# Kernel optimization log

Hardware: AMD Instinct MI355X
Metric: run time of the kernel (lower is better)

## Reference

```python
import jax, jax.numpy as jnp
import numpy as np

EPSILON = 0.3
ALPHA = 0.7
LN_EPS = 1e-5


def _layernorm(x, g, b):
    mu = jnp.mean(x, axis=-1, keepdims=True)
    var = jnp.mean((x - mu) ** 2, axis=-1, keepdims=True)
    return (x - mu) / jnp.sqrt(var + LN_EPS) * g + b


def setup_inputs() -> dict:
    key = jax.random.key(0)
    ks = jax.random.split(key, 6)
    B, N, D, L = 1, 2048, 768, 16
    s = 0.05  # weight scale to keep sigmoid/exp well-conditioned
    return {
        "x": jax.random.normal(ks[0], (B, N, D), jnp.float32),
        "proj_w": jax.random.normal(ks[1], (D, L), jnp.float32) * s,
        "proj_b": jnp.zeros((L,), jnp.float32),
        "ln1_g": jnp.ones((L,), jnp.float32),
        "ln1_b": jnp.zeros((L,), jnp.float32),
        "pi_w1": jax.random.normal(ks[2], (L, D), jnp.float32) * s,
        "pi_b1": jnp.zeros((D,), jnp.float32),
        "pi_w2": jax.random.normal(ks[3], (D, 1), jnp.float32) * s,
        "pi_b2": jnp.zeros((1,), jnp.float32),
        "dt": jnp.full((1,), 0.05, jnp.float32),
        "f_w": jax.random.normal(ks[4], (D, D), jnp.float32) * s,
        "f_b": jnp.zeros((D,), jnp.float32),
        "ln2_g": jnp.ones((D,), jnp.float32),
        "ln2_b": jnp.zeros((D,), jnp.float32),
    }


def reference(x, proj_w, proj_b, ln1_g, ln1_b, pi_w1, pi_b1, pi_w2, pi_b2, dt, f_w, f_b, ln2_g, ln2_b):
    B, N, D = x.shape
    # proj_list: Linear -> LayerNorm -> ReLU. [B,N,L]
    x_proj = jax.nn.relu(_layernorm(x @ proj_w + proj_b, ln1_g, ln1_b))
    # RBF kernel over pairwise differences. [B,N,N]
    diff = x_proj[:, :, None, :] - x_proj[:, None, :, :]
    K_eps = jnp.exp(-(1.0 / (4.0 * EPSILON)) * jnp.sum(diff * diff, axis=-1))
    q_tilde = jnp.sum(K_eps, axis=2)  # [B,N]
    # pi_list: Linear -> ReLU -> Linear -> Sigmoid. [B,N]
    pi = jax.nn.sigmoid(jax.nn.relu(x_proj @ pi_w1 + pi_b1) @ pi_w2 + pi_b2)[..., 0]
    v = pi / q_tilde  # diagonal of D_epsilon_tilde
    # K_tilde = K_eps @ diag(v): column scaling (math-equivalent to bmm with diag_embed)
    K_tilde = K_eps * v[:, None, :]
    d = jnp.sum(K_tilde, axis=2) + 1e-5  # diagonal of D_tilde
    # inv(D_tilde) @ K_tilde: row scaling; then subtract identity
    L_op = (1.0 / EPSILON) * (K_tilde / d[:, :, None]) - jnp.eye(N, dtype=x.dtype)[None]
    L_mat = L_op[0]  # .squeeze(0), B == 1
    # f(x): modeled as linear map
    target = x @ f_w + f_b  # [B,N,D]
    tt = dt * jnp.einsum('ij,bjd->bid', L_mat, target)  # target_transformed
    target1 = target + tt
    target2 = ALPHA * x + (1.0 - ALPHA) * (target1 + tt)
    return _layernorm(target2, ln2_g, ln2_b)
```

## Files before the change

kernel.cpp:

```cpp
#include <hip/hip_runtime.h>
#include <math.h>

#define EPSILON 0.3f
#define ALPHA 0.7f
#define LN_EPS 1e-5f

typedef __bf16 bf16x8 __attribute__((ext_vector_type(8)));
typedef float f32x4 __attribute__((ext_vector_type(4)));

__device__ __forceinline__ unsigned short f2bf(float f) {
  unsigned int u = __float_as_uint(f);
  return (unsigned short)((u + 0x7fffu + ((u >> 16) & 1u)) >> 16);
}
__device__ __forceinline__ unsigned int pack2(float lo, float hi) {
  return (unsigned int)f2bf(lo) | ((unsigned int)f2bf(hi) << 16);
}

__device__ __forceinline__ void async16(const unsigned short* g,
                                        unsigned short* l) {
  __builtin_amdgcn_global_load_lds(
      (const __attribute__((address_space(1))) unsigned int*)g,
      (__attribute__((address_space(3))) unsigned int*)l, 16, 0, 0);
}

__device__ __forceinline__ float wave_reduce(float v) {
#pragma unroll
  for (int off = 32; off > 0; off >>= 1) v += __shfl_xor(v, off, 64);
  return v;
}

__device__ __forceinline__ float blk_reduce_sum(float v, float* red) {
  v = wave_reduce(v);
  int lane = threadIdx.x & 63, wid = threadIdx.x >> 6;
  __syncthreads();
  if (lane == 0) red[wid] = v;
  __syncthreads();
  float s = 0.f;
  int nw = (blockDim.x + 63) >> 6;
  for (int w = 0; w < nw; ++w) s += red[w];
  return s;
}

__global__ __launch_bounds__(256) void k_proj(
    const float* __restrict__ x, const float* __restrict__ proj_w,
    const float* __restrict__ proj_b, const float* __restrict__ ln1_g,
    const float* __restrict__ ln1_b, const float* __restrict__ pi_w1,
    const float* __restrict__ pi_b1, const float* __restrict__ pi_w2,
    const float* __restrict__ pi_b2, const float* __restrict__ fw,
    unsigned short* __restrict__ fwTb, float* __restrict__ xp,
    float* __restrict__ s, float* __restrict__ pi, int N, int D) {
  __shared__ float xs[16][68];
  __shared__ float ws[64][20];
  __shared__ float ysh[16][17];
  __shared__ float xps[16][16];
  __shared__ float pr[16][4];
  int tid = threadIdx.x;
  int nProj = N / 16;
  if (blockIdx.x >= (unsigned)nProj) {
    unsigned short(*tile)[33] = (unsigned short(*)[33])&ws[0][0];
    int t = blockIdx.x - nProj;
    int tx = tid & 31, ty = tid >> 5;
    int cols = D / 32;
    int c0 = (t % cols) * 32, r0 = (t / cols) * 32;
#pragma unroll
    for (int i = 0; i < 4; ++i) {
      int r = r0 + ty + i * 8;
      tile[ty + i * 8][tx] = f2bf(fw[(size_t)r * D + c0 + tx]);
    }
    __syncthreads();
#pragma unroll
    for (int i = 0; i < 4; ++i) {
      int cc = c0 + ty + i * 8;
      fwTb[(size_t)cc * D + r0 + tx] = tile[tx][ty + i * 8];
    }
    return;
  }
  int row0 = blockIdx.x * 16;
  int row = tid >> 4, l = tid & 15;
  int lane = tid & 63, w = tid >> 6;
  int skc = (tid & 15) * 4;
  int wk = tid >> 2, wl = (tid & 3) * 4;
  float acc = 0.f;
  for (int k0 = 0; k0 < D; k0 += 64) {
    float4 xv = *(const float4*)(x + (size_t)(row0 + row) * D + k0 + skc);
    float4 wv = *(const float4*)(proj_w + (size_t)(k0 + wk) * 16 + wl);
    __syncthreads();
    *(float4*)&xs[row][skc] = xv;
    *(float4*)&ws[wk][wl] = wv;
    __syncthreads();
#pragma unroll
    for (int kk = 0; kk < 64; kk += 4) {
      float4 a4 = *(const float4*)&xs[row][kk];
      acc += a4.x * ws[kk + 0][l];
      acc += a4.y * ws[kk + 1][l];
      acc += a4.z * ws[kk + 2][l];
      acc += a4.w * ws[kk + 3][l];
    }
  }
  float y = acc + proj_b[l];
  ysh[row][l] = y;
  __syncthreads();
  float mu = 0.f;
#pragma unroll
  for (int t = 0; t < 16; ++t) mu += ysh[row][t];
  mu *= (1.f / 16.f);
  float var = 0.f;
#pragma unroll
  for (int t = 0; t < 16; ++t) { float d2 = ysh[row][t] - mu; var += d2 * d2; }
  var *= (1.f / 16.f);
  float rstd = rsqrtf(var + LN_EPS);
  float xpv = fmaxf((y - mu) * rstd * ln1_g[l] + ln1_b[l], 0.f);
  xps[row][l] = xpv;
  xp[(size_t)(row0 + row) * 16 + l] = xpv;
  float sq = xpv * xpv;
  sq += __shfl_xor(sq, 8, 64);
  sq += __shfl_xor(sq, 4, 64);
  sq += __shfl_xor(sq, 2, 64);
  sq += __shfl_xor(sq, 1, 64);
  if ((lane & 15) == 0) s[row0 + row] = sq;
  __syncthreads();
  float w1r[3][16], b1r[3], w2r[3];
#pragma unroll
  for (int c = 0; c < 3; ++c) {
    int d0 = tid + c * 256;
    b1r[c] = pi_b1[d0];
    w2r[c] = pi_w2[d0];
#pragma unroll
    for (int t = 0; t < 16; ++t) w1r[c][t] = pi_w1[(size_t)t * D + d0];
  }
  float pacc[16];
#pragma unroll
  for (int r = 0; r < 16; ++r) pacc[r] = 0.f;
#pragma unroll
  for (int r = 0; r < 16; ++r) {
    float xv[16];
#pragma unroll
    for (int t4 = 0; t4 < 4; ++t4) {
      float4 xq = *(const float4*)&xps[r][t4 * 4];
      xv[t4 * 4 + 0] = xq.x; xv[t4 * 4 + 1] = xq.y;
      xv[t4 * 4 + 2] = xq.z; xv[t4 * 4 + 3] = xq.w;
    }
    float pa = 0.f;
#pragma unroll
    for (int c = 0; c < 3; ++c) {
      float h = b1r[c];
#pragma unroll
      for (int t = 0; t < 16; ++t) h += xv[t] * w1r[c][t];
      h = fmaxf(h, 0.f);
      pa += h * w2r[c];
    }
    pacc[r] = pa;
  }
#pragma unroll
  for (int r = 0; r < 16; ++r) {
    float pv = wave_reduce(pacc[r]);
    if (lane == 0) pr[r][w] = pv;
  }
  __syncthreads();
  if (tid < 16) {
    float tot = pr[tid][0] + pr[tid][1] + pr[tid][2] + pr[tid][3] + pi_b2[0];
    pi[row0 + tid] = 1.f / (1.f + expf(-tot));
  }
}

__global__ __launch_bounds__(256) void k_keps(
    const float* __restrict__ xp, const float* __restrict__ s,
    const float* __restrict__ pi, unsigned short* __restrict__ Kb,
    float* __restrict__ v, int N) {
  __shared__ float qs[4][4];
  int i0 = blockIdx.x * 4;
  int tid = threadIdx.x, lane = tid & 63, w = tid >> 6;
  float a[4][16], si[4];
#pragma unroll
  for (int r = 0; r < 4; ++r) {
    const float* ap = xp + (size_t)(i0 + r) * 16;
#pragma unroll
    for (int t = 0; t < 16; ++t) a[r][t] = ap[t];
    si[r] = s[i0 + r];
  }
  const float c = 1.f / (4.f * EPSILON);
  float qa[4] = {0.f, 0.f, 0.f, 0.f};
  for (int it = 0; it < N / 512; ++it) {
    int j = it * 512 + tid * 2;
    const float4* bp = (const float4*)(xp + (size_t)j * 16);
    float4 b0 = bp[0], b1 = bp[1], b2 = bp[2], b3 = bp[3];
    float4 c0 = bp[4], c1 = bp[5], c2 = bp[6], c3 = bp[7];
    float bv[16] = {b0.x, b0.y, b0.z, b0.w, b1.x, b1.y, b1.z, b1.w,
                    b2.x, b2.y, b2.z, b2.w, b3.x, b3.y, b3.z, b3.w};
    float cv[16] = {c0.x, c0.y, c0.z, c0.w, c1.x, c1.y, c1.z, c1.w,
                    c2.x, c2.y, c2.z, c2.w, c3.x, c3.y, c3.z, c3.w};
    float sj0 = s[j], sj1 = s[j + 1];
#pragma unroll
    for (int r = 0; r < 4; ++r) {
      float d0 = 0.f, d1 = 0.f;
#pragma unroll
      for (int t = 0; t < 16; ++t) { d0 += a[r][t] * bv[t]; d1 += a[r][t] * cv[t]; }
      float k0 = expf(-c * (si[r] + sj0 - 2.f * d0));
      float k1 = expf(-c * (si[r] + sj1 - 2.f * d1));
      *(unsigned int*)(Kb + (size_t)(i0 + r) * N + j) = pack2(k0, k1);
      qa[r] += k0 + k1;
    }
  }
#pragma unroll
  for (int r = 0; r < 4; ++r) {
    float t = wave_reduce(qa[r]);
    if (lane == 0) qs[r][w] = t;
  }
  __syncthreads();
  if (tid < 4) {
    float tot = qs[tid][0] + qs[tid][1] + qs[tid][2] + qs[tid][3];
    v[i0 + tid] = pi[i0 + tid] / tot;
  }
}

__global__ __launch_bounds__(256) void k_prep(
    const unsigned short* __restrict__ Kb, const float* __restrict__ v,
    float* __restrict__ dv, const float* __restrict__ x,
    unsigned short* __restrict__ xvbT, int N, int D) {
  __shared__ float sh[544];
  int bid = blockIdx.x, tid = threadIdx.x;
  if (bid < N) {
    int i = bid;
    float acc = 0.f;
    for (int j8 = tid * 8; j8 < N; j8 += 256 * 8) {
      uint4 kv4 = *(const uint4*)(Kb + (size_t)i * N + j8);
      float4 va = *(const float4*)(v + j8);
      float4 vb = *(const float4*)(v + j8 + 4);
      unsigned int u;
      u = kv4.x;
      acc += __uint_as_float(u << 16) * va.x + __uint_as_float(u & 0xffff0000u) * va.y;
      u = kv4.y;
      acc += __uint_as_float(u << 16) * va.z + __uint_as_float(u & 0xffff0000u) * va.w;
      u = kv4.z;
      acc += __uint_as_float(u << 16) * vb.x + __uint_as_float(u & 0xffff0000u) * vb.y;
      u = kv4.w;
      acc += __uint_as_float(u << 16) * vb.z + __uint_as_float(u & 0xffff0000u) * vb.w;
    }
    float tot = blk_reduce_sum(acc, sh);
    if (tid == 0) dv[i] = tot + 1e-5f;
  } else {
    int t = bid - N;
    unsigned short(*tile)[33] = (unsigned short(*)[33])sh;
    int tx = tid & 31, ty = tid >> 5;
    int cols = D / 32;
    int c0 = (t % cols) * 32;
    int r0 = (t / cols) * 32;
#pragma unroll
    for (int i = 0; i < 4; ++i) {
      int r = r0 + ty + i * 8;
      tile[ty + i * 8][tx] = f2bf(v[r] * x[(size_t)r * D + c0 + tx]);
    }
    __syncthreads();
#pragma unroll
    for (int i = 0; i < 4; ++i) {
      int cc = c0 + ty + i * 8;
      xvbT[(size_t)cc * N + r0 + tx] = tile[tx][ty + i * 8];
    }
  }
}

#define GEMM_KLOOP(Aptr, Bptr, Kdim)                                          \
  int tid = threadIdx.x;                                                      \
  int w = tid >> 6, l = tid & 63;                                             \
  int ln = l & 15, quad = l >> 4;                                             \
  int mh = (w & 1) * 32, nh = (w >> 1) * 32;                                  \
  int row0 = blockIdx.y * 64, col0 = blockIdx.x * 64;                         \
  int sr = l >> 3, sj = l & 7;                                                \
  int swz = (sj ^ sr) * 8;                                                    \
  const unsigned short* gA0 = Aptr + (size_t)(row0 + w * 8 + sr) * Kdim + swz;\
  const unsigned short* gB0 = Bptr + (size_t)(col0 + w * 8 + sr) * Kdim + swz;\
  const unsigned short* gA1 = gA0 + (size_t)32 * Kdim;                        \
  const unsigned short* gB1 = gB0 + (size_t)32 * Kdim;                        \
  unsigned short* lA0 = As + w * 8 * 64;                                      \
  unsigned short* lA1 = As + (32 + w * 8) * 64;                               \
  unsigned short* lB0 = Bs + w * 8 * 64;                                      \
  unsigned short* lB1 = Bs + (32 + w * 8) * 64;                               \
  f32x4 acc[2][2] = {};                                                       \
  for (int k0 = 0; k0 < Kdim; k0 += 64) {                                     \
    __syncthreads();                                                          \
    async16(gA0 + k0, lA0);                                                   \
    async16(gA1 + k0, lA1);                                                   \
    async16(gB0 + k0, lB0);                                                   \
    async16(gB1 + k0, lB1);                                                   \
    __syncthreads();                                                          \
    _Pragma("unroll")                                                         \
    for (int ks = 0; ks < 2; ++ks) {                                          \
      bf16x8 bfr[2], afr[2];                                                  \
      _Pragma("unroll")                                                       \
      for (int nt = 0; nt < 2; ++nt) {                                        \
        int r = nh + nt * 16 + ln;                                            \
        int cix = (ks * 4 + quad) ^ (r & 7);                                  \
        bfr[nt] = *(const bf16x8*)&Bs[r * 64 + cix * 8];                      \
      }                                                                       \
      _Pragma("unroll")                                                       \
      for (int mt = 0; mt < 2; ++mt) {                                        \
        int r = mh + mt * 16 + ln;                                            \
        int cix = (ks * 4 + quad) ^ (r & 7);                                  \
        afr[mt] = *(const bf16x8*)&As[r * 64 + cix * 8];                      \
      }                                                                       \
      _Pragma("unroll")                                                       \
      for (int mt = 0; mt < 2; ++mt)                                          \
        _Pragma("unroll")                                                     \
        for (int nt = 0; nt < 2; ++nt)                                        \
          acc[mt][nt] = __builtin_amdgcn_mfma_f32_16x16x32_bf16(              \
              afr[mt], bfr[nt], acc[mt][nt], 0, 0, 0);                        \
    }                                                                         \
  }

__global__ __launch_bounds__(256) void k_gemmA(
    const unsigned short* __restrict__ A, const unsigned short* __restrict__ Bt,
    const float* __restrict__ x, const float* __restrict__ dv,
    const float* __restrict__ dtp, unsigned short* __restrict__ Z,
    int M, int N, int K) {
  __shared__ unsigned short As[64 * 64];
  __shared__ unsigned short Bs[64 * 64];
  GEMM_KLOOP(A, Bt, K)
  float dtv = dtp[0];
  float c2 = (1.f - ALPHA) * (1.f - 2.f * dtv);
  float c3b = (1.f - ALPHA) * 2.f * dtv / EPSILON;
#pragma unroll
  for (int mt = 0; mt < 2; ++mt)
#pragma unroll
    for (int nt = 0; nt < 2; ++nt) {
      int col = col0 + nh + nt * 16 + ln;
#pragma unroll
      for (int r = 0; r < 4; ++r) {
        int row = row0 + mh + mt * 16 + quad * 4 + r;
        float c3 = c3b / dv[row];
        Z[(size_t)row * N + col] =
            f2bf(c2 * x[(size_t)row * N + col] + c3 * acc[mt][nt][r]);
      }
    }
}

__global__ __launch_bounds__(256) void k_gemmB(
    const unsigned short* __restrict__ A, const unsigned short* __restrict__ Bt,
    const float* __restrict__ x, const float* __restrict__ bias,
    const float* __restrict__ dtp, float* __restrict__ out,
    int M, int N, int K) {
  __shared__ unsigned short As[64 * 64];
  __shared__ unsigned short Bs[64 * 64];
  GEMM_KLOOP(A, Bt, K)
  float dtv = dtp[0];
  float cb = (1.f - ALPHA) * (1.f - 2.f * dtv) +
             (1.f - ALPHA) * 2.f * dtv / EPSILON;
#pragma unroll
  for (int mt = 0; mt < 2; ++mt)
#pragma unroll
    for (int nt = 0; nt < 2; ++nt) {
      int col = col0 + nh + nt * 16 + ln;
      float bv = cb * bias[col];
#pragma unroll
      for (int r = 0; r < 4; ++r) {
        int row = row0 + mh + mt * 16 + quad * 4 + r;
        size_t idx = (size_t)row * N + col;
        out[idx] = ALPHA * x[idx] + acc[mt][nt][r] + bv;
      }
    }
}

__global__ __launch_bounds__(256) void k_ln_rows(
    float* __restrict__ out, const float* __restrict__ g,
    const float* __restrict__ b, int D) {
  __shared__ float red[4];
  int i = blockIdx.x, tid = threadIdx.x;
  float vv[4];
  int nt = D / 256;
  float sum = 0.f;
  for (int t = 0; t < nt; ++t) {
    vv[t] = out[(size_t)i * D + tid + t * 256];
    sum += vv[t];
  }
  float mu = blk_reduce_sum(sum, red) / (float)D;
  float sq = 0.f;
  for (int t = 0; t < nt; ++t) { float d2 = vv[t] - mu; sq += d2 * d2; }
  float var = blk_reduce_sum(sq, red) / (float)D;
  float rs = rsqrtf(var + LN_EPS);
  for (int t = 0; t < nt; ++t) {
    int d0 = tid + t * 256;
    out[(size_t)i * D + d0] = (vv[t] - mu) * rs * g[d0] + b[d0];
  }
}

extern "C" void kernel_launch(void* const* d_in, const int* in_sizes, int n_in,
                              void* d_out, int out_size, void* d_ws, size_t ws_size,
                              hipStream_t stream) {
  const float* x = (const float*)d_in[0];
  const float* proj_w = (const float*)d_in[1];
  const float* proj_b = (const float*)d_in[2];
  const float* ln1_g = (const float*)d_in[3];
  const float* ln1_b = (const float*)d_in[4];
  const float* pi_w1 = (const float*)d_in[5];
  const float* pi_b1 = (const float*)d_in[6];
  const float* pi_w2 = (const float*)d_in[7];
  const float* pi_b2 = (const float*)d_in[8];
  const float* dt = (const float*)d_in[9];
  const float* f_w = (const float*)d_in[10];
  const float* f_b = (const float*)d_in[11];
  const float* ln2_g = (const float*)d_in[12];
  const float* ln2_b = (const float*)d_in[13];
  float* out = (float*)d_out;

  int D = in_sizes[11];
  int N = in_sizes[0] / D;

  unsigned short* Kb = (unsigned short*)d_ws;
  unsigned short* xvbT = Kb + (size_t)N * N;
  unsigned short* fwTb = xvbT + (size_t)D * N;
  unsigned short* Z = fwTb + (size_t)D * D;
  float* xp = (float*)(Z + (size_t)N * D);
  float* s = xp + (size_t)N * 16;
  float* pi = s + N;
  float* v = pi + N;
  float* dv = v + N;

  int fwB = (D / 32) * (D / 32);
  int xvtB = (D / 32) * (N / 32);

  k_proj<<<N / 16 + fwB, 256, 0, stream>>>(x, proj_w, proj_b, ln1_g, ln1_b,
                                           pi_w1, pi_b1, pi_w2, pi_b2, f_w,
                                           fwTb, xp, s, pi, N, D);
  k_keps<<<N / 4, 256, 0, stream>>>(xp, s, pi, Kb, v, N);
  k_prep<<<N + xvtB, 256, 0, stream>>>(Kb, v, dv, x, xvbT, N, D);
  k_gemmA<<<dim3(D / 64, N / 64), 256, 0, stream>>>(Kb, xvbT, x, dv, dt, Z,
                                                    N, D, N);
  k_gemmB<<<dim3(D / 64, N / 64), 256, 0, stream>>>(Z, fwTb, x, f_b, dt, out,
                                                    N, D, D);
  k_ln_rows<<<N, 256, 0, stream>>>(out, ln2_g, ln2_b, D);
}
```

Before: 159.4 us.

## Double GEMM K-tile to 128, use fast exp, and simplify reductions

The GEMM k-loop now stages 128-wide K tiles, with a 16-way XOR swizzle and four async loads per thread. This halves the number of barrier pairs per output tile at the cost of twice the LDS per block. The RBF kernel switches from expf to __expf, trading a little accuracy for cheaper exponentials. It also fuses the pi partial-sum loop with its wave reduction and hardcodes the block reduction to four waves, which assumes 256-thread blocks.

Result: no change. 157.9 us, median of 2 (-1.0%).

```diff
diff --git a/kernel.cpp b/kernel.cpp
--- a/kernel.cpp
+++ b/kernel.cpp
@@ -35,10 +35,7 @@
   __syncthreads();
   if (lane == 0) red[wid] = v;
   __syncthreads();
-  float s = 0.f;
-  int nw = (blockDim.x + 63) >> 6;
-  for (int w = 0; w < nw; ++w) s += red[w];
-  return s;
+  return red[0] + red[1] + red[2] + red[3];
 }
 
 __global__ __launch_bounds__(256) void k_proj(
@@ -128,9 +125,6 @@
 #pragma unroll
     for (int t = 0; t < 16; ++t) w1r[c][t] = pi_w1[(size_t)t * D + d0];
   }
-  float pacc[16];
-#pragma unroll
-  for (int r = 0; r < 16; ++r) pacc[r] = 0.f;
 #pragma unroll
   for (int r = 0; r < 16; ++r) {
     float xv[16];
@@ -149,11 +143,7 @@
       h = fmaxf(h, 0.f);
       pa += h * w2r[c];
     }
-    pacc[r] = pa;
-  }
-#pragma unroll
-  for (int r = 0; r < 16; ++r) {
-    float pv = wave_reduce(pacc[r]);
+    float pv = wave_reduce(pa);
     if (lane == 0) pr[r][w] = pv;
   }
   __syncthreads();
@@ -195,8 +185,8 @@
       float d0 = 0.f, d1 = 0.f;
 #pragma unroll
       for (int t = 0; t < 16; ++t) { d0 += a[r][t] * bv[t]; d1 += a[r][t] * cv[t]; }
-      float k0 = expf(-c * (si[r] + sj0 - 2.f * d0));
-      float k1 = expf(-c * (si[r] + sj1 - 2.f * d1));
+      float k0 = __expf(-c * (si[r] + sj0 - 2.f * d0));
+      float k1 = __expf(-c * (si[r] + sj1 - 2.f * d1));
       *(unsigned int*)(Kb + (size_t)(i0 + r) * N + j) = pack2(k0, k1);
       qa[r] += k0 + k1;
     }
@@ -265,38 +255,33 @@
   int ln = l & 15, quad = l >> 4;                                             \
   int mh = (w & 1) * 32, nh = (w >> 1) * 32;                                  \
   int row0 = blockIdx.y * 64, col0 = blockIdx.x * 64;                         \
-  int sr = l >> 3, sj = l & 7;                                                \
-  int swz = (sj ^ sr) * 8;                                                    \
-  const unsigned short* gA0 = Aptr + (size_t)(row0 + w * 8 + sr) * Kdim + swz;\
-  const unsigned short* gB0 = Bptr + (size_t)(col0 + w * 8 + sr) * Kdim + swz;\
-  const unsigned short* gA1 = gA0 + (size_t)32 * Kdim;                        \
-  const unsigned short* gB1 = gB0 + (size_t)32 * Kdim;                        \
-  unsigned short* lA0 = As + w * 8 * 64;                                      \
-  unsigned short* lA1 = As + (32 + w * 8) * 64;                               \
-  unsigned short* lB0 = Bs + w * 8 * 64;                                      \
-  unsigned short* lB1 = Bs + (32 + w * 8) * 64;                               \
+  int srow = w * 4 + (l >> 4);                                                \
+  int swz = ((l & 15) ^ srow) * 8;                                            \
+  const unsigned short* gA = Aptr + (size_t)(row0 + srow) * Kdim + swz;       \
+  const unsigned short* gB = Bptr + (size_t)(col0 + srow) * Kdim + swz;       \
   f32x4 acc[2][2] = {};                                                       \
-  for (int k0 = 0; k0 < Kdim; k0 += 64) {                                     \
-    __syncthreads();                                                          \
-    async16(gA0 + k0, lA0);                                                   \
-    async16(gA1 + k0, lA1);                                                   \
-    async16(gB0 + k0, lB0);                                                   \
-    async16(gB1 + k0, lB1);                                                   \
+  for (int k0 = 0; k0 < Kdim; k0 += 128) {                                    \
     __syncthreads();                                                          \
     _Pragma("unroll")                                                         \
-    for (int ks = 0; ks < 2; ++ks) {                                          \
+    for (int q = 0; q < 4; ++q) {                                             \
+      async16(gA + (size_t)q * 16 * Kdim + k0, As + (q * 16 + w * 4) * 128);  \
+      async16(gB + (size_t)q * 16 * Kdim + k0, Bs + (q * 16 + w * 4) * 128);  \
+    }                                                                         \
+    __syncthreads();                                                          \
+    _Pragma("unroll")                                                         \
+    for (int ks = 0; ks < 4; ++ks) {                                          \
       bf16x8 bfr[2], afr[2];                                                  \
       _Pragma("unroll")                                                       \
       for (int nt = 0; nt < 2; ++nt) {                                        \
         int r = nh + nt * 16 + ln;                                            \
-        int cix = (ks * 4 + quad) ^ (r & 7);                                  \
-        bfr[nt] = *(const bf16x8*)&Bs[r * 64 + cix * 8];                      \
+        int cix = (ks * 4 + quad) ^ (r & 15);                                 \
+        bfr[nt] = *(const bf16x8*)&Bs[r * 128 + cix * 8];                     \
       }                                                                       \
       _Pragma("unroll")                                                       \
       for (int mt = 0; mt < 2; ++mt) {                                        \
         int r = mh + mt * 16 + ln;                                            \
-        int cix = (ks * 4 + quad) ^ (r & 7);                                  \
-        afr[mt] = *(const bf16x8*)&As[r * 64 + cix * 8];                      \
+        int cix = (ks * 4 + quad) ^ (r & 15);                                 \
+        afr[mt] = *(const bf16x8*)&As[r * 128 + cix * 8];                     \
       }                                                                       \
       _Pragma("unroll")                                                       \
       for (int mt = 0; mt < 2; ++mt)                                          \
@@ -312,8 +297,8 @@
     const float* __restrict__ x, const float* __restrict__ dv,
     const float* __restrict__ dtp, unsigned short* __restrict__ Z,
     int M, int N, int K) {
-  __shared__ unsigned short As[64 * 64];
-  __shared__ unsigned short Bs[64 * 64];
+  __shared__ unsigned short As[64 * 128];
+  __shared__ unsigned short Bs[64 * 128];
   GEMM_KLOOP(A, Bt, K)
   float dtv = dtp[0];
   float c2 = (1.f - ALPHA) * (1.f - 2.f * dtv);
@@ -338,8 +323,8 @@
     const float* __restrict__ x, const float* __restrict__ bias,
     const float* __restrict__ dtp, float* __restrict__ out,
     int M, int N, int K) {
-  __shared__ unsigned short As[64 * 64];
-  __shared__ unsigned short Bs[64 * 64];
+  __shared__ unsigned short As[64 * 128];
+  __shared__ unsigned short Bs[64 * 128];
   GEMM_KLOOP(A, Bt, K)
   float dtv = dtp[0];
   float cb = (1.f - ALPHA) * (1.f - 2.f * dtv) +
```
